# Optimization experiments

Measured on AMD Instinct MI355X. Metric: run time of the kernel, lower is better.

Reference implementation:

```python
import jax, jax.numpy as jnp
import numpy as np

N_NODES = 50000
N_REL = 4
N_EDGES = 800000
D_IN = 128
D_OUT = 128


def setup_inputs() -> dict:
    key = jax.random.key(0)
    ks = jax.random.split(key, 9)
    features = jax.random.normal(ks[0], (N_NODES, D_IN), dtype=jnp.float32)
    edge_index = jax.random.randint(ks[1], (N_REL, 2, N_EDGES), 0, N_NODES, dtype=jnp.int64)
    edge_weights = jax.random.uniform(ks[2], (N_REL, N_EDGES), dtype=jnp.float32)
    s_in = 1.0 / np.sqrt(D_IN)
    s_out = 1.0 / np.sqrt(D_OUT)
    Wr = jax.random.normal(ks[3], (N_REL, D_IN, D_OUT), dtype=jnp.float32) * s_in
    br = jax.random.normal(ks[4], (N_REL, D_OUT), dtype=jnp.float32) * s_in
    Wrw = jax.random.normal(ks[5], (D_IN, N_REL), dtype=jnp.float32) * s_in
    brw = jax.random.normal(ks[6], (N_REL,), dtype=jnp.float32) * s_in
    Wg = jax.random.normal(ks[7], (D_OUT, D_OUT), dtype=jnp.float32) * s_out
    bg = jax.random.normal(ks[8], (D_OUT,), dtype=jnp.float32) * s_out
    return {"features": features, "edge_index": edge_index, "edge_weights": edge_weights,
            "Wr": Wr, "br": br, "Wrw": Wrw, "brw": brw, "Wg": Wg, "bg": bg}


def reference(features, edge_index, edge_weights, Wr, br, Wrw, brw, Wg, bg):
    num_nodes = features.shape[0]
    num_rel = Wr.shape[0]
    # per-node softmax over relations  [N, R]
    rel_w = jax.nn.softmax(features @ Wrw + brw, axis=-1)
    combined = jnp.zeros((num_nodes, Wr.shape[2]), dtype=features.dtype)
    # small fixed loop over relations; edge dim fully vectorized
    for i in range(num_rel):
        src = features[edge_index[i, 0]]                      # gather  [E, D_in]
        msg = (src @ Wr[i] + br[i]) * edge_weights[i][:, None]  # [E, D_out]
        agg = jax.ops.segment_sum(msg, edge_index[i, 1], num_segments=num_nodes)
        combined = combined + rel_w[:, i:i + 1] * agg
    gate = jax.nn.sigmoid(combined @ Wg + bg)
    return gate * combined
```

## Files before the change

kernel.cpp:

```cpp
#include <hip/hip_runtime.h>
#include <hip/hip_fp16.h>

#define NN 50000
#define NR 4
#define NE 800000
#define DD 128
#define NSEG (NR * NN)
#define SCHUNK 1024
#define NCHUNK ((NSEG + SCHUNK - 1) / SCHUNK)

#define NXCD 8
#define DSLICE (NN / NXCD)
#define CBLK 1563

__global__ __launch_bounds__(256) void count_kernel(
    const int* __restrict__ eidx, int* __restrict__ cnt) {
  int xcd = blockIdx.x & (NXCD - 1);
  int vb = blockIdx.x >> 3;
  int lo = xcd * DSLICE, hi = lo + DSLICE;
  for (int idx = vb * 256 + threadIdx.x; idx < NR * NE; idx += CBLK * 256) {
    int r = idx / NE, e = idx - r * NE;
    int dst = eidx[(size_t)r * 2 * NE + NE + e];
    if (dst >= lo && dst < hi) atomicAdd(&cnt[r * NN + dst], 1);
  }
}

__global__ __launch_bounds__(256) void scan_local(
    const int* __restrict__ cnt, int* __restrict__ off,
    int* __restrict__ partial) {
  __shared__ int lds[256];
  int base = blockIdx.x * SCHUNK, t = threadIdx.x;
  int v[4], s = 0;
#pragma unroll
  for (int j = 0; j < 4; ++j) {
    int i = base + t * 4 + j;
    v[j] = (i < NSEG) ? cnt[i] : 0;
    s += v[j];
  }
  lds[t] = s;
  __syncthreads();
  for (int d = 1; d < 256; d <<= 1) {
    int x = (t >= d) ? lds[t - d] : 0;
    __syncthreads();
    lds[t] += x;
    __syncthreads();
  }
  int excl = (t == 0) ? 0 : lds[t - 1];
  if (t == 255) partial[blockIdx.x] = lds[255];
#pragma unroll
  for (int j = 0; j < 4; ++j) {
    int i = base + t * 4 + j;
    if (i < NSEG) off[i] = excl;
    excl += v[j];
  }
}

__global__ __launch_bounds__(256) void scan_partials(int* __restrict__ partial) {
  __shared__ int lds[256];
  int t = threadIdx.x;
  int v = (t < NCHUNK) ? partial[t] : 0;
  lds[t] = v;
  __syncthreads();
  for (int d = 1; d < 256; d <<= 1) {
    int x = (t >= d) ? lds[t - d] : 0;
    __syncthreads();
    lds[t] += x;
    __syncthreads();
  }
  int excl = (t == 0) ? 0 : lds[t - 1];
  if (t < NCHUNK) partial[t] = excl;
}

__global__ __launch_bounds__(256) void scan_add(
    int* __restrict__ off, const int* __restrict__ partial,
    int* __restrict__ off_run) {
  int base = blockIdx.x * SCHUNK;
  int add = partial[blockIdx.x];
  for (int j = threadIdx.x; j < SCHUNK; j += 256) {
    int i = base + j;
    if (i < NSEG) {
      int o = off[i] + add;
      off[i] = o;
      off_run[i] = o;
    }
  }
}

__global__ __launch_bounds__(256) void place_kernel(
    const int* __restrict__ eidx, const float* __restrict__ ew,
    int* __restrict__ off_run, int2* __restrict__ s_rec) {
  int xcd = blockIdx.x & (NXCD - 1);
  int vb = blockIdx.x >> 3;
  int lo = xcd * DSLICE, hi = lo + DSLICE;
  for (int idx = vb * 256 + threadIdx.x; idx < NR * NE; idx += CBLK * 256) {
    int r = idx / NE, e = idx - r * NE;
    int dst = eidx[(size_t)r * 2 * NE + NE + e];
    if (dst >= lo && dst < hi) {
      int src = eidx[(size_t)r * 2 * NE + e];
      float w = ew[(size_t)r * NE + e];
      int pos = atomicAdd(&off_run[r * NN + dst], 1);
      long long rec =
          (long long)(unsigned int)src | ((long long)__float_as_uint(w) << 32);
      __builtin_nontemporal_store(rec,
                                  reinterpret_cast<long long*>(s_rec + pos));
    }
  }
}

__global__ __launch_bounds__(256) void m_kernel(
    const float* __restrict__ feat, const float* __restrict__ Wr,
    __half* __restrict__ M) {
  __shared__ float wlds[DD * DD];
  __shared__ float flds[8][DD];
  int r = blockIdx.y;
  const float* W = Wr + (size_t)r * DD * DD;
  for (int i = threadIdx.x; i < DD * DD / 4; i += 256)
    reinterpret_cast<float4*>(wlds)[i] = reinterpret_cast<const float4*>(W)[i];
  int dgrp = threadIdx.x & 31, nl = threadIdx.x >> 5;
  int nbase = blockIdx.x * 128;
  for (int s = 0; s < 16; ++s) {
    int n0 = nbase + s * 8;
    __syncthreads();
    {
      int n = n0 + nl;
      float4 fv = make_float4(0.f, 0.f, 0.f, 0.f);
      if (n < NN) fv = reinterpret_cast<const float4*>(feat + (size_t)n * DD)[dgrp];
      reinterpret_cast<float4*>(&flds[nl][0])[dgrp] = fv;
    }
    __syncthreads();
    int n = n0 + nl;
    float4 acc = make_float4(0.f, 0.f, 0.f, 0.f);
#pragma unroll 8
    for (int k = 0; k < DD; ++k) {
      float f = flds[nl][k];
      float4 wv = reinterpret_cast<const float4*>(&wlds[k * DD])[dgrp];
      acc.x += f * wv.x; acc.y += f * wv.y;
      acc.z += f * wv.z; acc.w += f * wv.w;
    }
    if (n < NN) {
      __half2 h01 = __floats2half2_rn(acc.x, acc.y);
      __half2 h23 = __floats2half2_rn(acc.z, acc.w);
      __half2* mp = reinterpret_cast<__half2*>(
          M + ((size_t)r * NN + n) * DD + 4 * dgrp);
      mp[0] = h01;
      mp[1] = h23;
    }
  }
}

__global__ __launch_bounds__(256) void gather_y(
    const __half* __restrict__ M, const int2* __restrict__ s_rec,
    const int* __restrict__ off, const int* __restrict__ cnt,
    const float* __restrict__ feat, const float* __restrict__ Wrw,
    const float* __restrict__ brw, const float* __restrict__ br,
    float* __restrict__ y) {
  int wave = threadIdx.x >> 6, lane = threadIdx.x & 63;
  int n = blockIdx.x * 4 + wave;
  if (n >= NN) return;

  int l_r = lane >> 4, l_j = lane & 15;
  int l_seg = l_r * NN + n;
  int l_start = off[l_seg];
  int l_deg = cnt[l_seg];
  int pre_s = 0;
  float pre_w = 0.f;
  if (l_j < l_deg) {
    long long rr = __builtin_nontemporal_load(
        reinterpret_cast<const long long*>(s_rec + l_start + l_j));
    pre_s = (int)(unsigned int)rr;
    pre_w = __uint_as_float((unsigned int)((unsigned long long)rr >> 32));
  }

  float rwv[4];
  {
    float2 f = reinterpret_cast<const float2*>(feat + (size_t)n * DD)[lane];
    float4 w0 = reinterpret_cast<const float4*>(Wrw)[2 * lane];
    float4 w1 = reinterpret_cast<const float4*>(Wrw)[2 * lane + 1];
    float a0 = f.x * w0.x + f.y * w1.x;
    float a1 = f.x * w0.y + f.y * w1.y;
    float a2 = f.x * w0.z + f.y * w1.z;
    float a3 = f.x * w0.w + f.y * w1.w;
    for (int o = 32; o; o >>= 1) {
      a0 += __shfl_xor(a0, o);
      a1 += __shfl_xor(a1, o);
      a2 += __shfl_xor(a2, o);
      a3 += __shfl_xor(a3, o);
    }
    a0 += brw[0]; a1 += brw[1]; a2 += brw[2]; a3 += brw[3];
    float m = fmaxf(fmaxf(a0, a1), fmaxf(a2, a3));
    float e0 = __expf(a0 - m), e1 = __expf(a1 - m);
    float e2 = __expf(a2 - m), e3 = __expf(a3 - m);
    float inv = 1.f / (e0 + e1 + e2 + e3);
    rwv[0] = e0 * inv; rwv[1] = e1 * inv; rwv[2] = e2 * inv; rwv[3] = e3 * inv;
  }

  float2 acc = make_float2(0.f, 0.f);
#pragma unroll
  for (int r = 0; r < NR; ++r) {
    int start = __shfl(l_start, r << 4);
    int deg = __shfl(l_deg, r << 4);
    const __half2* mbase =
        reinterpret_cast<const __half2*>(M + (size_t)r * NN * DD);
    float2 pacc = make_float2(0.f, 0.f);
    float sw = 0.f;
    int nbat = (deg + 15) >> 4;
    int cur_s = pre_s;
    float cur_w = pre_w;
    int sb = r << 4;
    for (int b = 0; b < nbat; ++b) {
      int nxt_s = 0;
      float nxt_w = 0.f;
      int nbase = (b + 1) << 4;
      if (nbase < deg && lane < 16) {
        int idx2 = nbase + lane;
        if (idx2 < deg) {
          long long rr = __builtin_nontemporal_load(
              reinterpret_cast<const long long*>(s_rec + start + idx2));
          nxt_s = (int)(unsigned int)rr;
          nxt_w = __uint_as_float((unsigned int)((unsigned long long)rr >> 32));
        }
      }
#pragma unroll
      for (int j = 0; j < 16; ++j) {
        int s = __shfl(cur_s, sb + j);
        float w = __shfl(cur_w, sb + j);
        float2 mf = __half22float2(mbase[(size_t)s * 64 + lane]);
        pacc.x += w * mf.x;
        pacc.y += w * mf.y;
        sw += w;
      }
      cur_s = nxt_s;
      cur_w = nxt_w;
      sb = 0;
    }
    float2 bv = reinterpret_cast<const float2*>(br + (size_t)r * DD)[lane];
    float rw = rwv[r];
    acc.x += rw * (pacc.x + sw * bv.x);
    acc.y += rw * (pacc.y + sw * bv.y);
  }
  reinterpret_cast<float2*>(y + (size_t)n * DD)[lane] = acc;
}

__global__ __launch_bounds__(256) void gate_kernel(
    float* __restrict__ out, const float* __restrict__ Wg,
    const float* __restrict__ bg) {
  __shared__ float wlds[DD * DD];
  __shared__ float clds[8][DD];
  for (int i = threadIdx.x; i < DD * DD / 4; i += 256)
    reinterpret_cast<float4*>(wlds)[i] = reinterpret_cast<const float4*>(Wg)[i];
  int dgrp = threadIdx.x & 31, nl = threadIdx.x >> 5;
  float4 bv = reinterpret_cast<const float4*>(bg)[dgrp];
  int nbase = blockIdx.x * 128;
  for (int s = 0; s < 16; ++s) {
    int n0 = nbase + s * 8;
    __syncthreads();
    {
      int n = n0 + nl;
      float4 cv = make_float4(0.f, 0.f, 0.f, 0.f);
      if (n < NN) cv = reinterpret_cast<const float4*>(out + (size_t)n * DD)[dgrp];
      reinterpret_cast<float4*>(&clds[nl][0])[dgrp] = cv;
    }
    __syncthreads();
    int n = n0 + nl;
    float4 acc = bv;
#pragma unroll 8
    for (int k = 0; k < DD; ++k) {
      float c = clds[nl][k];
      float4 wv = reinterpret_cast<const float4*>(&wlds[k * DD])[dgrp];
      acc.x += c * wv.x; acc.y += c * wv.y;
      acc.z += c * wv.z; acc.w += c * wv.w;
    }
    if (n < NN) {
      float4 cv = reinterpret_cast<float4*>(&clds[nl][0])[dgrp];
      float4 res;
      res.x = cv.x / (1.f + __expf(-acc.x));
      res.y = cv.y / (1.f + __expf(-acc.y));
      res.z = cv.z / (1.f + __expf(-acc.z));
      res.w = cv.w / (1.f + __expf(-acc.w));
      reinterpret_cast<float4*>(out + (size_t)n * DD)[dgrp] = res;
    }
  }
}

extern "C" void kernel_launch(void* const* d_in, const int* in_sizes, int n_in,
                              void* d_out, int out_size, void* d_ws,
                              size_t ws_size, hipStream_t stream) {
  const float* feat = (const float*)d_in[0];
  const int* eidx   = (const int*)d_in[1];
  const float* ew   = (const float*)d_in[2];
  const float* Wr   = (const float*)d_in[3];
  const float* br   = (const float*)d_in[4];
  const float* Wrw  = (const float*)d_in[5];
  const float* brw  = (const float*)d_in[6];
  const float* Wg   = (const float*)d_in[7];
  const float* bg   = (const float*)d_in[8];
  float* out = (float*)d_out;

  char* p = (char*)d_ws;
  int2*   s_rec  = (int2*)p;   p += (size_t)NR * NE * 8;
  int*    cnt    = (int*)p;    p += (size_t)NSEG * 4;
  int*    off    = (int*)p;    p += (size_t)NSEG * 4;
  int*    offrun = (int*)p;    p += (size_t)NSEG * 4;
  int*    part   = (int*)p;    p += 4096;
  __half* M      = (__half*)p; p += (size_t)NR * NN * DD * 2;

  hipMemsetAsync(cnt, 0, (size_t)NSEG * 4, stream);

  count_kernel<<<NXCD * CBLK, 256, 0, stream>>>(eidx, cnt);
  scan_local<<<NCHUNK, 256, 0, stream>>>(cnt, off, part);
  scan_partials<<<1, 256, 0, stream>>>(part);
  scan_add<<<NCHUNK, 256, 0, stream>>>(off, part, offrun);
  place_kernel<<<NXCD * CBLK, 256, 0, stream>>>(eidx, ew, offrun, s_rec);
  m_kernel<<<dim3((NN + 127) / 128, NR), 256, 0, stream>>>(feat, Wr, M);
  gather_y<<<(NN + 3) / 4, 256, 0, stream>>>(M, s_rec, off, cnt, feat, Wrw,
                                             brw, br, out);
  gate_kernel<<<(NN + 127) / 128, 256, 0, stream>>>(out, Wg, bg);
}
```

Before: 736.5 us.

## Compute per-relation feature transform with fp16 MFMA instead of scalar FMA

```diff
diff --git a/kernel.cpp b/kernel.cpp
--- a/kernel.cpp
+++ b/kernel.cpp
@@ -12,6 +12,9 @@
 #define NXCD 8
 #define DSLICE (NN / NXCD)
 #define CBLK 1563
+
+typedef _Float16 f16x8 __attribute__((ext_vector_type(8)));
+typedef float f32x4 __attribute__((ext_vector_type(4)));
 
 __global__ __launch_bounds__(256) void count_kernel(
     const int* __restrict__ eidx, int* __restrict__ cnt) {
@@ -110,40 +113,50 @@
 __global__ __launch_bounds__(256) void m_kernel(
     const float* __restrict__ feat, const float* __restrict__ Wr,
     __half* __restrict__ M) {
-  __shared__ float wlds[DD * DD];
-  __shared__ float flds[8][DD];
+  __shared__ __half wt[DD * DD];
   int r = blockIdx.y;
   const float* W = Wr + (size_t)r * DD * DD;
-  for (int i = threadIdx.x; i < DD * DD / 4; i += 256)
-    reinterpret_cast<float4*>(wlds)[i] = reinterpret_cast<const float4*>(W)[i];
-  int dgrp = threadIdx.x & 31, nl = threadIdx.x >> 5;
-  int nbase = blockIdx.x * 128;
-  for (int s = 0; s < 16; ++s) {
-    int n0 = nbase + s * 8;
-    __syncthreads();
-    {
-      int n = n0 + nl;
-      float4 fv = make_float4(0.f, 0.f, 0.f, 0.f);
-      if (n < NN) fv = reinterpret_cast<const float4*>(feat + (size_t)n * DD)[dgrp];
-      reinterpret_cast<float4*>(&flds[nl][0])[dgrp] = fv;
-    }
-    __syncthreads();
-    int n = n0 + nl;
-    float4 acc = make_float4(0.f, 0.f, 0.f, 0.f);
-#pragma unroll 8
-    for (int k = 0; k < DD; ++k) {
-      float f = flds[nl][k];
-      float4 wv = reinterpret_cast<const float4*>(&wlds[k * DD])[dgrp];
-      acc.x += f * wv.x; acc.y += f * wv.y;
-      acc.z += f * wv.z; acc.w += f * wv.w;
-    }
-    if (n < NN) {
-      __half2 h01 = __floats2half2_rn(acc.x, acc.y);
-      __half2 h23 = __floats2half2_rn(acc.z, acc.w);
-      __half2* mp = reinterpret_cast<__half2*>(
-          M + ((size_t)r * NN + n) * DD + 4 * dgrp);
-      mp[0] = h01;
-      mp[1] = h23;
+  char* wtb = reinterpret_cast<char*>(wt);
+  for (int i = threadIdx.x; i < DD * DD; i += 256) {
+    int k = i >> 7, c = i & 127;
+    int bo = (c * 256 + k * 2) ^ ((c & 7) << 4);
+    *reinterpret_cast<_Float16*>(wtb + bo) = (_Float16)W[i];
+  }
+  __syncthreads();
+
+  int wv = threadIdx.x >> 6, l = threadIdx.x & 63;
+  int n0 = blockIdx.x * 64 + wv * 16;
+  int arow = n0 + (l & 15);
+  int kgrp = (l >> 4) * 8;
+  const float* fr = feat + (size_t)(arow < NN ? arow : 0) * DD;
+
+  f32x4 acc[8] = {};
+  for (int k0 = 0; k0 < DD; k0 += 32) {
+    float4 fa = *reinterpret_cast<const float4*>(fr + k0 + kgrp);
+    float4 fb = *reinterpret_cast<const float4*>(fr + k0 + kgrp + 4);
+    f16x8 a;
+    a[0] = (_Float16)fa.x; a[1] = (_Float16)fa.y;
+    a[2] = (_Float16)fa.z; a[3] = (_Float16)fa.w;
+    a[4] = (_Float16)fb.x; a[5] = (_Float16)fb.y;
+    a[6] = (_Float16)fb.z; a[7] = (_Float16)fb.w;
+#pragma unroll
+    for (int c = 0; c < 8; ++c) {
+      int col = c * 16 + (l & 15);
+      int bo = (col * 256 + (k0 + kgrp) * 2) ^ ((col & 7) << 4);
+      f16x8 b = *reinterpret_cast<const f16x8*>(wtb + bo);
+      acc[c] = __builtin_amdgcn_mfma_f32_16x16x32_f16(a, b, acc[c], 0, 0, 0);
+    }
+  }
+
+  int rbase = n0 + 4 * (l >> 4);
+  __half* Mr = M + (size_t)r * NN * DD;
+#pragma unroll
+  for (int c = 0; c < 8; ++c) {
+    int col = c * 16 + (l & 15);
+#pragma unroll
+    for (int j = 0; j < 4; ++j) {
+      int row = rbase + j;
+      if (row < NN) Mr[(size_t)row * DD + col] = __float2half(acc[c][j]);
     }
   }
 }
@@ -311,7 +324,7 @@
   scan_partials<<<1, 256, 0, stream>>>(part);
   scan_add<<<NCHUNK, 256, 0, stream>>>(off, part, offrun);
   place_kernel<<<NXCD * CBLK, 256, 0, stream>>>(eidx, ew, offrun, s_rec);
-  m_kernel<<<dim3((NN + 127) / 128, NR), 256, 0, stream>>>(feat, Wr, M);
+  m_kernel<<<dim3((NN + 63) / 64, NR), 256, 0, stream>>>(feat, Wr, M);
   gather_y<<<(NN + 3) / 4, 256, 0, stream>>>(M, s_rec, off, cnt, feat, Wrw,
                                              brw, br, out);
   gate_kernel<<<(NN + 127) / 128, 256, 0, stream>>>(out, Wg, bg);
```

New measurement: 603.8 us. -18.0%, faster.
